# Performance work log

Measured on AMD Instinct MI355X. Metric: run time of the kernel, lower is better.

The kernel has to match this reference:

```python
import jax, jax.numpy as jnp
import numpy as np

N_NODES, N_EDGES, N_LAYERS, N_CH, N_GRAPHS = 50000, 1600000, 4, 16, 64
HID = N_CH * 3  # 16x1o -> dim 48

_eps = np.zeros((3, 3, 3), dtype=np.float32)
_eps[0, 1, 2] = _eps[1, 2, 0] = _eps[2, 0, 1] = 1.0
_eps[0, 2, 1] = _eps[2, 1, 0] = _eps[1, 0, 2] = -1.0
EPS = jnp.asarray(_eps)  # Levi-Civita: CG coeffs for 1 (x) 1 -> 1
TP_NORM = 1.0 / np.sqrt(2.0 * N_CH).astype(np.float32)  # CG norm * path fan-in norm


def setup_inputs():
    key = jax.random.key(0)
    ks = jax.random.split(key, 12)
    return {
        "x": jax.random.normal(ks[0], (N_NODES, 3), jnp.float32),
        "edge_index": jax.random.randint(ks[1], (2, N_EDGES), 0, N_NODES, jnp.int32),
        "edge_attr": jax.random.normal(ks[2], (N_EDGES, 5), jnp.float32),
        "batch": jnp.sort(jax.random.randint(ks[3], (N_NODES,), 0, N_GRAPHS, jnp.int32)),
        "embed_w": jax.random.normal(ks[4], (3, HID), jnp.float32) * 0.3,
        "mlp1_w": jax.random.normal(ks[5], (N_LAYERS, 3, 16), jnp.float32) * 0.5,
        "mlp1_b": jnp.zeros((N_LAYERS, 16), jnp.float32),
        "mlp2_w": jax.random.normal(ks[6], (N_LAYERS, 16, HID), jnp.float32) * 0.25,
        "mlp2_b": jnp.zeros((N_LAYERS, HID), jnp.float32),
        "tp_w": jax.random.normal(ks[7], (N_LAYERS, N_CH, N_CH), jnp.float32),
        "lin_w": jax.random.normal(ks[8], (HID, 1), jnp.float32) * 0.1,
        "lin_b": jnp.zeros((1,), jnp.float32),
    }


def reference(x, edge_index, edge_attr, batch, embed_w, mlp1_w, mlp1_b,
              mlp2_w, mlp2_b, tp_w, lin_w, lin_b):
    n = x.shape[0]
    e = edge_attr.shape[0]
    src, dst = edge_index[0], edge_index[1]

    h = x @ embed_w  # [N, 48] node embedding

    r_ij = edge_attr[:, 2:5]                            # [E, 3]
    r2 = jnp.sum(r_ij * r_ij, axis=-1, keepdims=True)   # [E, 1]
    rhat = r_ij / jnp.maximum(jnp.sqrt(r2), 1e-12)
    sh = jnp.sqrt(3.0) * rhat                            # l=1 SH, component norm
    edge_scalar = jnp.concatenate([edge_attr[:, 0:2], r2], axis=-1)  # [E, 3]

    for l in range(N_LAYERS):
        gate = jax.nn.silu(edge_scalar @ mlp1_w[l] + mlp1_b[l]) @ mlp2_w[l] + mlp2_b[l]  # [E,48]
        xj = h[src].reshape(e, N_CH, 3)                  # gather neighbor feats
        # fully-connected tensor product 16x1o (x) 1o -> 16x1o (cross-product CG)
        tp = jnp.einsum('kij,eui,ej,uv->evk', EPS, xj, sh, tp_w[l]) * TP_NORM
        msg = gate * tp.reshape(e, HID)
        dx = jax.ops.segment_sum(msg, dst, num_segments=n)  # scatter-add
        h = h + dx  # residual

    sums = jax.ops.segment_sum(h, batch, num_segments=N_GRAPHS)
    cnt = jax.ops.segment_sum(jnp.ones((n,), h.dtype), batch, num_segments=N_GRAPHS)
    pooled = sums / jnp.maximum(cnt, 1.0)[:, None]       # global mean pool
    return (pooled @ lin_w + lin_b).ravel()              # [B]
```

## Files before the change

### kernel.cpp

```cpp
#include <hip/hip_runtime.h>

#define N_NODES 50000
#define N_EDGES 1600000
#define N_LAYERS 4
#define N_CH 16
#define HID 48
#define N_GRAPHS 64
#define TP_NORM 0.17677669529663687f
#define SQRT3 1.7320508075688772f
#define REB 256
#define MPAD 28
#define NBLK (N_EDGES / REB)
#define NPART ((N_NODES + 255) / 256)

typedef float v2f __attribute__((ext_vector_type(2)));

__device__ __forceinline__ unsigned bfpack2(float a, float b) {
    unsigned ua = __float_as_uint(a);
    unsigned ub = __float_as_uint(b);
    ua = (ua + 0x7fffu + ((ua >> 16) & 1u)) >> 16;
    ub = (ub + 0x7fffu + ((ub >> 16) & 1u)) >> 16;
    return ua | (ub << 16);
}
#define BFLO(u) __uint_as_float((u) << 16)
#define BFHI(u) __uint_as_float((u) & 0xffff0000u)

__global__ void k_embed(const float* __restrict__ x, const float* __restrict__ ew,
                        float* __restrict__ h) {
    int t = blockIdx.x * blockDim.x + threadIdx.x;
    if (t >= N_NODES * HID) return;
    int n = t / HID, c = t % HID;
    h[t] = x[n * 3 + 0] * ew[c] + x[n * 3 + 1] * ew[HID + c] + x[n * 3 + 2] * ew[2 * HID + c];
}

__global__ void k_count(const int* __restrict__ ei, unsigned* __restrict__ cnt32,
                        unsigned char* __restrict__ rank8,
                        const float* __restrict__ x, const float* __restrict__ ew,
                        float* __restrict__ h) {
    int e = blockIdx.x * 256 + threadIdx.x;
    int d = ei[N_EDGES + e];
    int sh = 8 * (d & 3);
    unsigned old = atomicAdd(&cnt32[d >> 2], 1u << sh);
    rank8[e] = (unsigned char)((old >> sh) & 0xffu);
    for (int t = e; t < N_NODES * HID; t += N_EDGES) {
        int n = t / HID, c = t % HID;
        h[t] = x[n * 3 + 0] * ew[c] + x[n * 3 + 1] * ew[HID + c] + x[n * 3 + 2] * ew[2 * HID + c];
    }
}

__global__ void k_sred(const unsigned char* __restrict__ cnt8, int* __restrict__ bsum) {
    __shared__ int red[256];
    int b = blockIdx.x, t = threadIdx.x;
    int idx = b * 256 + t;
    red[t] = (idx < N_NODES) ? (int)cnt8[idx] : 0;
    __syncthreads();
    for (int d = 128; d > 0; d >>= 1) {
        if (t < d) red[t] += red[t + d];
        __syncthreads();
    }
    if (t == 0) bsum[b] = red[0];
}

__global__ void k_sscan(const int* __restrict__ bsum, int* __restrict__ bbase) {
    __shared__ int s[256];
    int t = threadIdx.x;
    int v = (t < NPART) ? bsum[t] : 0;
    s[t] = v;
    __syncthreads();
    for (int d = 1; d < 256; d <<= 1) {
        int x = (t >= d) ? s[t - d] : 0;
        __syncthreads();
        s[t] += x;
        __syncthreads();
    }
    if (t < NPART) bbase[t] = s[t] - v;
    if (t == NPART - 1) bbase[NPART] = s[t];
}

__global__ void k_soff(const unsigned char* __restrict__ cnt8, const int* __restrict__ bbase,
                       int* __restrict__ off) {
    __shared__ int s[256];
    int b = blockIdx.x, t = threadIdx.x;
    int idx = b * 256 + t;
    int v = (idx < N_NODES) ? (int)cnt8[idx] : 0;
    s[t] = v;
    __syncthreads();
    for (int d = 1; d < 256; d <<= 1) {
        int x = (t >= d) ? s[t - d] : 0;
        __syncthreads();
        s[t] += x;
        __syncthreads();
    }
    if (idx < N_NODES) off[idx] = bbase[b] + s[t] - v;
    if (idx == 0) off[N_NODES] = bbase[NPART];
}

__global__ void k_rng(const int* __restrict__ off, int* __restrict__ blk) {
    int b = blockIdx.x * blockDim.x + threadIdx.x;
    if (b >= NBLK) return;
    int base = b * REB;
    int lo = 0, hi = N_NODES;
    while (lo < hi) { int mid = (lo + hi + 1) >> 1; if (off[mid] <= base) lo = mid; else hi = mid - 1; }
    blk[2 * b] = lo;
    int last = base + REB - 1;
    int hi2 = N_NODES;
    while (lo < hi2) { int mid = (lo + hi2 + 1) >> 1; if (off[mid] <= last) lo = mid; else hi2 = mid - 1; }
    blk[2 * b + 1] = lo;
}

__global__ void k_build(const int* __restrict__ ei, const float* __restrict__ ea,
                        const int* __restrict__ off, const unsigned char* __restrict__ rank8,
                        uint4* __restrict__ es_s) {
    int e = blockIdx.x * 256 + threadIdx.x;
    int d = ei[N_EDGES + e];
    int pos = off[d] + (int)rank8[e];
    float a0 = ea[e * 5 + 0], a1 = ea[e * 5 + 1];
    float rx = ea[e * 5 + 2], ry = ea[e * 5 + 3], rz = ea[e * 5 + 4];
    float r2 = rx * rx + ry * ry + rz * rz;
    float inv = rsqrtf(fmaxf(r2, 1e-24f)) * (SQRT3 * TP_NORM);
    uint4 o;
    o.x = bfpack2(a0, a1);
    o.y = bfpack2(r2, rx * inv);
    o.z = bfpack2(ry * inv, rz * inv);
    o.w = (unsigned)ei[e];
    es_s[pos] = o;
}

__global__ void k_h2(const float* __restrict__ hin, const float* __restrict__ tpw,
                     unsigned* __restrict__ h2, float* __restrict__ dx) {
    int t = blockIdx.x * blockDim.x + threadIdx.x;
    if (t >= N_NODES * 24) return;
    int n = t / 24, p = t % 24;
    int c0 = 2 * p, c1 = c0 + 1;
    int v0 = c0 / 3, i0 = c0 % 3;
    int v1 = c1 / 3, i1 = c1 % 3;
    const float* hr = hin + (size_t)n * HID;
    float s0 = 0.f, s1 = 0.f;
#pragma unroll
    for (int u = 0; u < 16; u++) {
        s0 = fmaf(tpw[u * 16 + v0], hr[u * 3 + i0], s0);
        s1 = fmaf(tpw[u * 16 + v1], hr[u * 3 + i1], s1);
    }
    h2[t] = bfpack2(s0, s1);
    *(float2*)(dx + (size_t)n * HID + c0) = make_float2(0.f, 0.f);
}

__global__ void k_h2_add(const float* __restrict__ hin, const float* __restrict__ dxin,
                         const float* __restrict__ tpw,
                         unsigned* __restrict__ h2, float* __restrict__ hout,
                         float* __restrict__ dxout) {
    int t = blockIdx.x * blockDim.x + threadIdx.x;
    if (t >= N_NODES * 24) return;
    int n = t / 24, p = t % 24;
    int c0 = 2 * p, c1 = c0 + 1;
    int v0 = c0 / 3, i0 = c0 % 3;
    int v1 = c1 / 3, i1 = c1 % 3;
    size_t rb = (size_t)n * HID;
    const float* hr = hin + rb;
    const float* dr = dxin + rb;
    float s0 = 0.f, s1 = 0.f;
#pragma unroll
    for (int u = 0; u < 16; u++) {
        float e0 = hr[u * 3 + i0] + dr[u * 3 + i0];
        float e1 = hr[u * 3 + i1] + dr[u * 3 + i1];
        s0 = fmaf(tpw[u * 16 + v0], e0, s0);
        s1 = fmaf(tpw[u * 16 + v1], e1, s1);
    }
    h2[t] = bfpack2(s0, s1);
    float2 hv = *(const float2*)(hr + c0);
    float2 dv = *(const float2*)(dr + c0);
    *(float2*)(hout + rb + c0) = make_float2(hv.x + dv.x, hv.y + dv.y);
    *(float2*)(dxout + rb + c0) = make_float2(0.f, 0.f);
}

__global__ void __launch_bounds__(256) k_fused(
    const uint4* __restrict__ es_s, const int* __restrict__ off,
    const int* __restrict__ blk,
    const unsigned* __restrict__ h2, float* __restrict__ dx,
    const float* __restrict__ m1w, const float* __restrict__ m1b,
    const float* __restrict__ m2w, const float* __restrict__ m2b)
{
    __shared__ float s_msg[REB][MPAD];

    int t = threadIdx.x;
    int base = blockIdx.x * REB;
    int e2 = base + t;

    uint4 rec = es_s[e2];
    int src = (int)rec.w;
    const uint4* hv = (const uint4*)(h2 + (size_t)src * 24);
    uint4 A0 = hv[0], A1 = hv[1], A2 = hv[2];
    int n0 = blk[2 * blockIdx.x];
    int n1 = blk[2 * blockIdx.x + 1];

    float a0 = BFLO(rec.x), a1 = BFHI(rec.x);
    float r2 = BFLO(rec.y), shx = BFHI(rec.y);
    float shy = BFLO(rec.z), shz = BFHI(rec.z);

    float hid[16];
#pragma unroll
    for (int j = 0; j < 16; j++) {
        float z = fmaf(a0, m1w[j], fmaf(a1, m1w[16 + j], fmaf(r2, m1w[32 + j], m1b[j])));
        hid[j] = z * __builtin_amdgcn_rcpf(1.f + __expf(-z));
    }

    int gid = t / 24;
    int rem = t % 24;
    int q    = rem >> 2;
    int quad = rem & 3;

    float xj[24];
#define UNPK8(u, d) { (d)[0]=BFLO((u).x); (d)[1]=BFHI((u).x); (d)[2]=BFLO((u).y); (d)[3]=BFHI((u).y); \
                      (d)[4]=BFLO((u).z); (d)[5]=BFHI((u).z); (d)[6]=BFLO((u).w); (d)[7]=BFHI((u).w); }
    UNPK8(A0, &xj[0]); UNPK8(A1, &xj[8]); UNPK8(A2, &xj[16]);

    alignas(16) v2f mv[12];
    float* m = (float*)mv;

#pragma unroll
    for (int qq = 0; qq < 6; qq++) {
        float4 b = *(const float4*)(m2b + qq * 4);
        mv[2 * qq + 0] = (v2f){b.x, b.y};
        mv[2 * qq + 1] = (v2f){b.z, b.w};
    }
#pragma unroll
    for (int j = 0; j < 16; j++) {
        v2f hj2 = (v2f){hid[j], hid[j]};
#pragma unroll
        for (int qq = 0; qq < 6; qq++) {
            float4 w4 = *(const float4*)(m2w + j * 48 + qq * 4);
            mv[2 * qq + 0] = __builtin_elementwise_fma(hj2, (v2f){w4.x, w4.y}, mv[2 * qq + 0]);
            mv[2 * qq + 1] = __builtin_elementwise_fma(hj2, (v2f){w4.z, w4.w}, mv[2 * qq + 1]);
        }
    }
#pragma unroll
    for (int v = 0; v < 8; v++) {
        float x0 = xj[v * 3 + 0], x1 = xj[v * 3 + 1], x2 = xj[v * 3 + 2];
        m[v * 3 + 0] *= x1 * shz - x2 * shy;
        m[v * 3 + 1] *= x2 * shx - x0 * shz;
        m[v * 3 + 2] *= x0 * shy - x1 * shx;
    }
    {
        float4* row = (float4*)&s_msg[t][0];
#pragma unroll
        for (int qq = 0; qq < 6; qq++) row[qq] = ((float4*)m)[qq];
    }
    {
        uint4 B0 = hv[3], B1 = hv[4], B2 = hv[5];
        UNPK8(B0, &xj[0]); UNPK8(B1, &xj[8]); UNPK8(B2, &xj[16]);
    }
    __syncthreads();

    if (t < 240) {
        for (int nn = n0 + gid; nn <= n1; nn += 10) {
            int lo = off[nn], hi = off[nn + 1];
            int rlo = (lo > base) ? lo - base : 0;
            int rhi = ((hi < base + REB) ? hi : base + REB) - base;
            if (rlo < rhi) {
                float4 acc = make_float4(0.f, 0.f, 0.f, 0.f);
                for (int r = rlo + quad; r < rhi; r += 4) {
                    float4 v = *(const float4*)&s_msg[r][q * 4];
                    acc.x += v.x; acc.y += v.y; acc.z += v.z; acc.w += v.w;
                }
                acc.x += __shfl_xor(acc.x, 1); acc.y += __shfl_xor(acc.y, 1);
                acc.z += __shfl_xor(acc.z, 1); acc.w += __shfl_xor(acc.w, 1);
                acc.x += __shfl_xor(acc.x, 2); acc.y += __shfl_xor(acc.y, 2);
                acc.z += __shfl_xor(acc.z, 2); acc.w += __shfl_xor(acc.w, 2);
                if (quad == 0) {
                    float* dp = dx + (size_t)nn * HID + q * 4;
                    if (lo < base || hi > base + REB) {
                        atomicAdd(dp + 0, acc.x); atomicAdd(dp + 1, acc.y);
                        atomicAdd(dp + 2, acc.z); atomicAdd(dp + 3, acc.w);
                    } else {
                        *(float4*)dp = acc;
                    }
                }
            }
        }
    }
    __syncthreads();

#pragma unroll
    for (int qq = 0; qq < 6; qq++) {
        float4 b = *(const float4*)(m2b + 24 + qq * 4);
        mv[2 * qq + 0] = (v2f){b.x, b.y};
        mv[2 * qq + 1] = (v2f){b.z, b.w};
    }
#pragma unroll
    for (int j = 0; j < 16; j++) {
        v2f hj2 = (v2f){hid[j], hid[j]};
#pragma unroll
        for (int qq = 0; qq < 6; qq++) {
            float4 w4 = *(const float4*)(m2w + j * 48 + 24 + qq * 4);
            mv[2 * qq + 0] = __builtin_elementwise_fma(hj2, (v2f){w4.x, w4.y}, mv[2 * qq + 0]);
            mv[2 * qq + 1] = __builtin_elementwise_fma(hj2, (v2f){w4.z, w4.w}, mv[2 * qq + 1]);
        }
    }
#pragma unroll
    for (int v = 0; v < 8; v++) {
        float x0 = xj[v * 3 + 0], x1 = xj[v * 3 + 1], x2 = xj[v * 3 + 2];
        m[v * 3 + 0] *= x1 * shz - x2 * shy;
        m[v * 3 + 1] *= x2 * shx - x0 * shz;
        m[v * 3 + 2] *= x0 * shy - x1 * shx;
    }
    {
        float4* row = (float4*)&s_msg[t][0];
#pragma unroll
        for (int qq = 0; qq < 6; qq++) row[qq] = ((float4*)m)[qq];
    }
    __syncthreads();

    if (t < 240) {
        for (int nn = n0 + gid; nn <= n1; nn += 10) {
            int lo = off[nn], hi = off[nn + 1];
            int rlo = (lo > base) ? lo - base : 0;
            int rhi = ((hi < base + REB) ? hi : base + REB) - base;
            if (rlo < rhi) {
                float4 acc = make_float4(0.f, 0.f, 0.f, 0.f);
                for (int r = rlo + quad; r < rhi; r += 4) {
                    float4 v = *(const float4*)&s_msg[r][q * 4];
                    acc.x += v.x; acc.y += v.y; acc.z += v.z; acc.w += v.w;
                }
                acc.x += __shfl_xor(acc.x, 1); acc.y += __shfl_xor(acc.y, 1);
                acc.z += __shfl_xor(acc.z, 1); acc.w += __shfl_xor(acc.w, 1);
                acc.x += __shfl_xor(acc.x, 2); acc.y += __shfl_xor(acc.y, 2);
                acc.z += __shfl_xor(acc.z, 2); acc.w += __shfl_xor(acc.w, 2);
                if (quad == 0) {
                    float* dp = dx + (size_t)nn * HID + 24 + q * 4;
                    if (lo < base || hi > base + REB) {
                        atomicAdd(dp + 0, acc.x); atomicAdd(dp + 1, acc.y);
                        atomicAdd(dp + 2, acc.z); atomicAdd(dp + 3, acc.w);
                    } else {
                        *(float4*)dp = acc;
                    }
                }
            }
        }
    }
}

__global__ void k_add(float* __restrict__ h, float* __restrict__ dx) {
    int t = blockIdx.x * blockDim.x + threadIdx.x;
    if (t >= N_NODES * HID) return;
    h[t] += dx[t];
    dx[t] = 0.f;
}

__global__ void __launch_bounds__(256) k_pool(
    const float* __restrict__ h, const float* __restrict__ dxin, const int* __restrict__ batch,
    const float* __restrict__ linw, float* __restrict__ gsum, float* __restrict__ gcnt)
{
    __shared__ float ss[N_GRAPHS];
    __shared__ float sc[N_GRAPHS];
    for (int i = threadIdx.x; i < N_GRAPHS; i += 256) { ss[i] = 0.f; sc[i] = 0.f; }
    __syncthreads();
    int n = blockIdx.x * 256 + threadIdx.x;
    if (n < N_NODES) {
        float s = 0.f;
        const float4* hv = (const float4*)(h + (size_t)n * HID);
        const float4* dv = (const float4*)(dxin + (size_t)n * HID);
#pragma unroll
        for (int qq = 0; qq < 12; qq++) {
            float4 v = hv[qq], d = dv[qq];
            s += (v.x + d.x) * linw[qq * 4 + 0] + (v.y + d.y) * linw[qq * 4 + 1]
               + (v.z + d.z) * linw[qq * 4 + 2] + (v.w + d.w) * linw[qq * 4 + 3];
        }
        int b = batch[n];
        atomicAdd(&ss[b], s);
        atomicAdd(&sc[b], 1.f);
    }
    __syncthreads();
    for (int i = threadIdx.x; i < N_GRAPHS; i += 256) {
        if (sc[i] != 0.f) {
            atomicAdd(&gsum[i], ss[i]);
            atomicAdd(&gcnt[i], sc[i]);
        }
    }
}

__global__ void k_final(const float* __restrict__ gsum, const float* __restrict__ gcnt,
                        const float* __restrict__ linb, float* __restrict__ out) {
    int g = threadIdx.x;
    if (g < N_GRAPHS) out[g] = gsum[g] / fmaxf(gcnt[g], 1.f) + linb[0];
}

__global__ void __launch_bounds__(256) k_edge_atomic(
    const int* __restrict__ ei, const float* __restrict__ ea,
    const float* __restrict__ h, float* __restrict__ dx,
    const float* __restrict__ m1w, const float* __restrict__ m1b,
    const float* __restrict__ m2w, const float* __restrict__ m2b,
    const float* __restrict__ tpw)
{
    __shared__ float s_m1w[48];
    __shared__ float s_m1b[16];
    __shared__ float s_m2w[768];
    __shared__ float s_m2b[48];
    __shared__ float s_tpw[256];
    for (int i = threadIdx.x; i < 48;  i += 256) s_m1w[i] = m1w[i];
    for (int i = threadIdx.x; i < 16;  i += 256) s_m1b[i] = m1b[i];
    for (int i = threadIdx.x; i < 768; i += 256) s_m2w[i] = m2w[i];
    for (int i = threadIdx.x; i < 48;  i += 256) s_m2b[i] = m2b[i];
    for (int i = threadIdx.x; i < 256; i += 256) s_tpw[i] = tpw[i];
    __syncthreads();
    int e = blockIdx.x * 256 + threadIdx.x;
    int src = ei[e];
    int dst = ei[N_EDGES + e];
    float a0 = ea[e * 5 + 0], a1 = ea[e * 5 + 1];
    float rx = ea[e * 5 + 2], ry = ea[e * 5 + 3], rz = ea[e * 5 + 4];
    float r2 = rx * rx + ry * ry + rz * rz;
    float inv = rsqrtf(fmaxf(r2, 1e-24f));
    float shx = SQRT3 * rx * inv, shy = SQRT3 * ry * inv, shz = SQRT3 * rz * inv;
    float hid[16];
#pragma unroll
    for (int j = 0; j < 16; j++) {
        float z = a0 * s_m1w[j] + a1 * s_m1w[16 + j] + r2 * s_m1w[32 + j] + s_m1b[j];
        hid[j] = z / (1.f + __expf(-z));
    }
    float xj[48];
    const float4* hv = (const float4*)(h + (size_t)src * HID);
#pragma unroll
    for (int qq = 0; qq < 12; qq++) {
        float4 v = hv[qq];
        xj[qq * 4 + 0] = v.x; xj[qq * 4 + 1] = v.y; xj[qq * 4 + 2] = v.z; xj[qq * 4 + 3] = v.w;
    }
    float cr[48];
#pragma unroll
    for (int u = 0; u < 16; u++) {
        float x0 = xj[u * 3 + 0], x1 = xj[u * 3 + 1], x2 = xj[u * 3 + 2];
        cr[u * 3 + 0] = x1 * shz - x2 * shy;
        cr[u * 3 + 1] = x2 * shx - x0 * shz;
        cr[u * 3 + 2] = x0 * shy - x1 * shx;
    }
    float* dd = dx + (size_t)dst * HID;
#pragma unroll
    for (int v = 0; v < 16; v++) {
        float t0 = 0.f, t1 = 0.f, t2 = 0.f;
#pragma unroll
        for (int u = 0; u < 16; u++) {
            float w = s_tpw[u * 16 + v];
            t0 += w * cr[u * 3 + 0];
            t1 += w * cr[u * 3 + 1];
            t2 += w * cr[u * 3 + 2];
        }
        float g0 = s_m2b[v * 3 + 0], g1 = s_m2b[v * 3 + 1], g2 = s_m2b[v * 3 + 2];
#pragma unroll
        for (int j = 0; j < 16; j++) {
            float hj = hid[j];
            g0 = fmaf(hj, s_m2w[j * 48 + v * 3 + 0], g0);
            g1 = fmaf(hj, s_m2w[j * 48 + v * 3 + 1], g1);
            g2 = fmaf(hj, s_m2w[j * 48 + v * 3 + 2], g2);
        }
        atomicAdd(dd + v * 3 + 0, g0 * t0 * TP_NORM);
        atomicAdd(dd + v * 3 + 1, g1 * t1 * TP_NORM);
        atomicAdd(dd + v * 3 + 2, g2 * t2 * TP_NORM);
    }
}

extern "C" void kernel_launch(void* const* d_in, const int* in_sizes, int n_in,
                              void* d_out, int out_size, void* d_ws, size_t ws_size,
                              hipStream_t stream) {
    const float* x    = (const float*)d_in[0];
    const int*   ei   = (const int*)  d_in[1];
    const float* ea   = (const float*)d_in[2];
    const int*   batch= (const int*)  d_in[3];
    const float* ew   = (const float*)d_in[4];
    const float* m1w  = (const float*)d_in[5];
    const float* m1b  = (const float*)d_in[6];
    const float* m2w  = (const float*)d_in[7];
    const float* m2b  = (const float*)d_in[8];
    const float* tpw  = (const float*)d_in[9];
    const float* linw = (const float*)d_in[10];
    const float* linb = (const float*)d_in[11];
    float* out = (float*)d_out;

    char* w = (char*)d_ws;
    auto alloc = [&](size_t bytes) -> char* {
        char* p = w;
        w += (bytes + 255) & ~(size_t)255;
        return p;
    };
    float*    hA   = (float*)   alloc((size_t)N_NODES * HID * 4);
    float*    hB   = (float*)   alloc((size_t)N_NODES * HID * 4);
    unsigned* h2   = (unsigned*)alloc((size_t)N_NODES * 24 * 4);
    float*    dxA  = (float*)   alloc((size_t)N_NODES * HID * 4);
    float*    dxB  = (float*)   alloc((size_t)N_NODES * HID * 4);
    float*    gbuf = (float*)   alloc(2 * N_GRAPHS * 4);
    uint4*    es_s = (uint4*)   alloc((size_t)N_EDGES * 16);
    int*      off  = (int*)     alloc((size_t)(N_NODES + 1) * 4);
    unsigned* cnt  = (unsigned*)alloc((size_t)((N_NODES + 3) / 4) * 4);
    unsigned char* rank8 = (unsigned char*)alloc((size_t)N_EDGES);
    int*      blk  = (int*)     alloc((size_t)NBLK * 2 * 4);
    int*      bsum = (int*)     alloc((size_t)NPART * 4);
    int*      bbase= (int*)     alloc((size_t)(NPART + 1) * 4);
    size_t need = (size_t)(w - (char*)d_ws);
    float* gsum = gbuf;
    float* gcnt = gbuf + N_GRAPHS;

    if (ws_size < need) {
        float* fh   = (float*)d_ws;
        float* fdx  = fh + (size_t)N_NODES * HID;
        float* fgs  = fdx + (size_t)N_NODES * HID;
        float* fgc  = fgs + N_GRAPHS;
        hipMemsetAsync(fdx, 0, ((size_t)N_NODES * HID + 2 * N_GRAPHS) * sizeof(float), stream);
        k_embed<<<(N_NODES * HID + 255) / 256, 256, 0, stream>>>(x, ew, fh);
        for (int l = 0; l < N_LAYERS; l++) {
            k_edge_atomic<<<N_EDGES / 256, 256, 0, stream>>>(ei, ea, fh, fdx,
                m1w + l * 48, m1b + l * 16, m2w + l * 768, m2b + l * 48, tpw + l * 256);
            k_add<<<(N_NODES * HID + 255) / 256, 256, 0, stream>>>(fh, fdx);
        }
        hipMemsetAsync(fdx, 0, (size_t)N_NODES * HID * 4, stream);
        k_pool<<<(N_NODES + 255) / 256, 256, 0, stream>>>(fh, fdx, batch, linw, fgs, fgc);
        k_final<<<1, 64, 0, stream>>>(fgs, fgc, linb, out);
        return;
    }

    hipMemsetAsync(cnt, 0, (size_t)((N_NODES + 3) / 4) * 4, stream);
    hipMemsetAsync(gbuf, 0, 2 * N_GRAPHS * 4, stream);
    k_count<<<N_EDGES / 256, 256, 0, stream>>>(ei, cnt, rank8, x, ew, hA);
    k_sred<<<NPART, 256, 0, stream>>>((const unsigned char*)cnt, bsum);
    k_sscan<<<1, 256, 0, stream>>>(bsum, bbase);
    k_soff<<<NPART, 256, 0, stream>>>((const unsigned char*)cnt, bbase, off);
    k_rng<<<(NBLK + 255) / 256, 256, 0, stream>>>(off, blk);
    k_build<<<N_EDGES / 256, 256, 0, stream>>>(ei, ea, off, rank8, es_s);

    const int npBlocks = (N_NODES * 24 + 255) / 256;
    float* dxs[2] = { dxA, dxB };
    float* hcur = hA;
    float* hnxt = hB;
    for (int l = 0; l < N_LAYERS; l++) {
        float* dxw = dxs[l & 1];
        if (l == 0) {
            k_h2<<<npBlocks, 256, 0, stream>>>(hcur, tpw, h2, dxw);
        } else {
            k_h2_add<<<npBlocks, 256, 0, stream>>>(hcur, dxs[(l - 1) & 1], tpw + l * 256,
                                                   h2, hnxt, dxw);
            float* tmp = hcur; hcur = hnxt; hnxt = tmp;
        }
        k_fused<<<NBLK, 256, 0, stream>>>(es_s, off, blk, h2, dxw,
            m1w + l * 48, m1b + l * 16, m2w + l * 768, m2b + l * 48);
    }

    k_pool<<<(N_NODES + 255) / 256, 256, 0, stream>>>(hcur, dxs[(N_LAYERS - 1) & 1],
                                                      batch, linw, gsum, gcnt);
    k_final<<<1, 64, 0, stream>>>(gsum, gcnt, linb, out);
}
```

Measured before the change: 426.2 us.

## Replace global-atomic degree count with per-block LDS histograms for CSR build

Edge counting by destination now uses per-block shared-memory packed byte histograms over contiguous edge chunks, written out per block. A column-scan kernel turns these into per-block prefix offsets and degrees. The build kernel then recomputes local ranks with shared atomics instead of reading a rank array. The goal is to cut contended global atomics and the rank8 traffic, at the cost of a 256x12.5K-word histogram buffer and a strided scan. Separately, the fused kernel now issues its second half of the neighbor-feature loads earlier so they overlap with the gate computation.

```diff
diff --git a/kernel.cpp b/kernel.cpp
--- a/kernel.cpp
+++ b/kernel.cpp
@@ -12,6 +12,10 @@
 #define MPAD 28
 #define NBLK (N_EDGES / REB)
 #define NPART ((N_NODES + 255) / 256)
+#define SBLK 256
+#define EPB (N_EDGES / SBLK)
+#define HW ((N_NODES + 3) / 4)
+#define HB (HW * 4)
 
 typedef float v2f __attribute__((ext_vector_type(2)));
 
@@ -33,26 +37,47 @@
     h[t] = x[n * 3 + 0] * ew[c] + x[n * 3 + 1] * ew[HID + c] + x[n * 3 + 2] * ew[2 * HID + c];
 }
 
-__global__ void k_count(const int* __restrict__ ei, unsigned* __restrict__ cnt32,
-                        unsigned char* __restrict__ rank8,
-                        const float* __restrict__ x, const float* __restrict__ ew,
-                        float* __restrict__ h) {
-    int e = blockIdx.x * 256 + threadIdx.x;
-    int d = ei[N_EDGES + e];
-    int sh = 8 * (d & 3);
-    unsigned old = atomicAdd(&cnt32[d >> 2], 1u << sh);
-    rank8[e] = (unsigned char)((old >> sh) & 0xffu);
-    for (int t = e; t < N_NODES * HID; t += N_EDGES) {
-        int n = t / HID, c = t % HID;
-        h[t] = x[n * 3 + 0] * ew[c] + x[n * 3 + 1] * ew[HID + c] + x[n * 3 + 2] * ew[2 * HID + c];
-    }
-}
-
-__global__ void k_sred(const unsigned char* __restrict__ cnt8, int* __restrict__ bsum) {
+__global__ void __launch_bounds__(512) k_hist1(
+    const int* __restrict__ ei, unsigned* __restrict__ hist32,
+    const float* __restrict__ x, const float* __restrict__ ew, float* __restrict__ h) {
+    __shared__ unsigned lh[HW];
+    int b = blockIdx.x, t = threadIdx.x;
+    for (int i = t; i < HW; i += 512) lh[i] = 0;
+    __syncthreads();
+    int e0 = b * EPB, e1 = e0 + EPB;
+    for (int e = e0 + t; e < e1; e += 512) {
+        int d = ei[N_EDGES + e];
+        atomicAdd(&lh[d >> 2], 1u << (8 * (d & 3)));
+    }
+    __syncthreads();
+    unsigned* gh = hist32 + (size_t)b * HW;
+    for (int i = t; i < HW; i += 512) gh[i] = lh[i];
+    int tid = b * 512 + t;
+    for (int i = tid; i < N_NODES * HID; i += SBLK * 512) {
+        int n = i / HID, c = i % HID;
+        h[i] = x[n * 3 + 0] * ew[c] + x[n * 3 + 1] * ew[HID + c] + x[n * 3 + 2] * ew[2 * HID + c];
+    }
+}
+
+__global__ void k_cscan(unsigned char* __restrict__ hist8, int* __restrict__ deg32) {
+    int d = blockIdx.x * 256 + threadIdx.x;
+    if (d >= N_NODES) return;
+    unsigned run = 0;
+    unsigned char* p = hist8 + d;
+#pragma unroll 8
+    for (int b = 0; b < SBLK; b++) {
+        unsigned v = p[(size_t)b * HB];
+        p[(size_t)b * HB] = (unsigned char)run;
+        run += v;
+    }
+    deg32[d] = (int)run;
+}
+
+__global__ void k_sred(const int* __restrict__ cnt, int* __restrict__ bsum) {
     __shared__ int red[256];
     int b = blockIdx.x, t = threadIdx.x;
     int idx = b * 256 + t;
-    red[t] = (idx < N_NODES) ? (int)cnt8[idx] : 0;
+    red[t] = (idx < N_NODES) ? cnt[idx] : 0;
     __syncthreads();
     for (int d = 128; d > 0; d >>= 1) {
         if (t < d) red[t] += red[t + d];
@@ -77,12 +102,12 @@
     if (t == NPART - 1) bbase[NPART] = s[t];
 }
 
-__global__ void k_soff(const unsigned char* __restrict__ cnt8, const int* __restrict__ bbase,
+__global__ void k_soff(const int* __restrict__ cnt, const int* __restrict__ bbase,
                        int* __restrict__ off) {
     __shared__ int s[256];
     int b = blockIdx.x, t = threadIdx.x;
     int idx = b * 256 + t;
-    int v = (idx < N_NODES) ? (int)cnt8[idx] : 0;
+    int v = (idx < N_NODES) ? cnt[idx] : 0;
     s[t] = v;
     __syncthreads();
     for (int d = 1; d < 256; d <<= 1) {
@@ -108,22 +133,33 @@
     blk[2 * b + 1] = lo;
 }
 
-__global__ void k_build(const int* __restrict__ ei, const float* __restrict__ ea,
-                        const int* __restrict__ off, const unsigned char* __restrict__ rank8,
-                        uint4* __restrict__ es_s) {
-    int e = blockIdx.x * 256 + threadIdx.x;
-    int d = ei[N_EDGES + e];
-    int pos = off[d] + (int)rank8[e];
-    float a0 = ea[e * 5 + 0], a1 = ea[e * 5 + 1];
-    float rx = ea[e * 5 + 2], ry = ea[e * 5 + 3], rz = ea[e * 5 + 4];
-    float r2 = rx * rx + ry * ry + rz * rz;
-    float inv = rsqrtf(fmaxf(r2, 1e-24f)) * (SQRT3 * TP_NORM);
-    uint4 o;
-    o.x = bfpack2(a0, a1);
-    o.y = bfpack2(r2, rx * inv);
-    o.z = bfpack2(ry * inv, rz * inv);
-    o.w = (unsigned)ei[e];
-    es_s[pos] = o;
+__global__ void __launch_bounds__(512) k_build2(
+    const int* __restrict__ ei, const float* __restrict__ ea,
+    const int* __restrict__ off, const unsigned char* __restrict__ hist8,
+    uint4* __restrict__ es_s) {
+    __shared__ unsigned lr[HW];
+    int b = blockIdx.x, t = threadIdx.x;
+    for (int i = t; i < HW; i += 512) lr[i] = 0;
+    __syncthreads();
+    int e0 = b * EPB, e1 = e0 + EPB;
+    const unsigned char* hb = hist8 + (size_t)b * HB;
+    for (int e = e0 + t; e < e1; e += 512) {
+        int d = ei[N_EDGES + e];
+        int sh = 8 * (d & 3);
+        unsigned old = atomicAdd(&lr[d >> 2], 1u << sh);
+        int local = (int)((old >> sh) & 0xffu);
+        int pos = off[d] + (int)hb[d] + local;
+        float a0 = ea[e * 5 + 0], a1 = ea[e * 5 + 1];
+        float rx = ea[e * 5 + 2], ry = ea[e * 5 + 3], rz = ea[e * 5 + 4];
+        float r2 = rx * rx + ry * ry + rz * rz;
+        float inv = rsqrtf(fmaxf(r2, 1e-24f)) * (SQRT3 * TP_NORM);
+        uint4 o;
+        o.x = bfpack2(a0, a1);
+        o.y = bfpack2(r2, rx * inv);
+        o.z = bfpack2(ry * inv, rz * inv);
+        o.w = (unsigned)ei[e];
+        es_s[pos] = o;
+    }
 }
 
 __global__ void k_h2(const float* __restrict__ hin, const float* __restrict__ tpw,
@@ -190,6 +226,7 @@
     int src = (int)rec.w;
     const uint4* hv = (const uint4*)(h2 + (size_t)src * 24);
     uint4 A0 = hv[0], A1 = hv[1], A2 = hv[2];
+    uint4 B0 = hv[3], B1 = hv[4], B2 = hv[5];
     int n0 = blk[2 * blockIdx.x];
     int n1 = blk[2 * blockIdx.x + 1];
 
@@ -245,10 +282,7 @@
 #pragma unroll
         for (int qq = 0; qq < 6; qq++) row[qq] = ((float4*)m)[qq];
     }
-    {
-        uint4 B0 = hv[3], B1 = hv[4], B2 = hv[5];
-        UNPK8(B0, &xj[0]); UNPK8(B1, &xj[8]); UNPK8(B2, &xj[16]);
-    }
+    UNPK8(B0, &xj[0]); UNPK8(B1, &xj[8]); UNPK8(B2, &xj[16]);
     __syncthreads();
 
     if (t < 240) {
@@ -487,8 +521,8 @@
     float*    gbuf = (float*)   alloc(2 * N_GRAPHS * 4);
     uint4*    es_s = (uint4*)   alloc((size_t)N_EDGES * 16);
     int*      off  = (int*)     alloc((size_t)(N_NODES + 1) * 4);
-    unsigned* cnt  = (unsigned*)alloc((size_t)((N_NODES + 3) / 4) * 4);
-    unsigned char* rank8 = (unsigned char*)alloc((size_t)N_EDGES);
+    unsigned* hist = (unsigned*)alloc((size_t)SBLK * HW * 4);
+    int*      deg  = (int*)     alloc((size_t)N_NODES * 4);
     int*      blk  = (int*)     alloc((size_t)NBLK * 2 * 4);
     int*      bsum = (int*)     alloc((size_t)NPART * 4);
     int*      bbase= (int*)     alloc((size_t)(NPART + 1) * 4);
@@ -514,14 +548,14 @@
         return;
     }
 
-    hipMemsetAsync(cnt, 0, (size_t)((N_NODES + 3) / 4) * 4, stream);
     hipMemsetAsync(gbuf, 0, 2 * N_GRAPHS * 4, stream);
-    k_count<<<N_EDGES / 256, 256, 0, stream>>>(ei, cnt, rank8, x, ew, hA);
-    k_sred<<<NPART, 256, 0, stream>>>((const unsigned char*)cnt, bsum);
+    k_hist1<<<SBLK, 512, 0, stream>>>(ei, hist, x, ew, hA);
+    k_cscan<<<(N_NODES + 255) / 256, 256, 0, stream>>>((unsigned char*)hist, deg);
+    k_sred<<<NPART, 256, 0, stream>>>(deg, bsum);
     k_sscan<<<1, 256, 0, stream>>>(bsum, bbase);
-    k_soff<<<NPART, 256, 0, stream>>>((const unsigned char*)cnt, bbase, off);
+    k_soff<<<NPART, 256, 0, stream>>>(deg, bbase, off);
     k_rng<<<(NBLK + 255) / 256, 256, 0, stream>>>(off, blk);
-    k_build<<<N_EDGES / 256, 256, 0, stream>>>(ei, ea, off, rank8, es_s);
+    k_build2<<<SBLK, 512, 0, stream>>>(ei, ea, off, (const unsigned char*)hist, es_s);
 
     const int npBlocks = (N_NODES * 24 + 255) / 256;
     float* dxs[2] = { dxA, dxB };
```

Result: faster. 379.7 us (median of 2 runs) (-10.9%).
